# Performance work log

Hardware: AMD Instinct MI355X
Metric: run time of the kernel (lower is better)

## Reference

```python
import jax, jax.numpy as jnp
import numpy as np

THRESH = 1.0
TAU_M = 20.0
TAU_S = 5.0
NUM_STEPS = 8
SCALE = 0.2
BATCH = 8
DM = np.float32(np.exp(-1.0 / TAU_M))
DS = np.float32(np.exp(-1.0 / TAU_S))


@jax.custom_vjp
def spike_fn(x):
    return (x > 0.0).astype(x.dtype)

def _sf_fwd(x):
    return (x > 0.0).astype(x.dtype), x

def _sf_bwd(x, g):
    # rectangular surrogate gradient (lens = 0.5), standard for NOSO/SNN training
    return (g * (jnp.abs(x) < 0.5).astype(x.dtype),)

spike_fn.defvjp(_sf_fwd, _sf_bwd)


def conv5x5(x, w):
    return jax.lax.conv_general_dilated(x, w, (1, 1), ((2, 2), (2, 2)),
                                        dimension_numbers=('NCHW', 'OIHW', 'NCHW'))


def noso_conv(w, in_sp, sav, vm, vs):
    # dual-exponential NOSO neuron: pre-synaptic traces vm/vs, membrane u = sav*(conv(vm)-conv(vs))
    vm = DM * vm + in_sp
    vs = DS * vs + in_sp
    um = conv5x5(vm, w)
    us = conv5x5(vs, w)
    u = sav * (um - us)
    sp = spike_fn(u - THRESH)
    sav = sav * (1.0 - sp)  # one spike per neuron
    return sav, vm, vs, um, u, sp


def noso_fc(w, in_sp, sav, vm, vs):
    vm = DM * vm + in_sp
    vs = DS * vs + in_sp
    um = jnp.einsum('bi,oi->bo', vm, w)
    us = jnp.einsum('bi,oi->bo', vs, w)
    u = sav * (um - us)
    sp = spike_fn(u - THRESH)
    sav = sav * (1.0 - sp)
    return sav, vm, vs, um, u, sp


def minpool(sp, lat):
    # latency-based 2x2 min-pool: pass through the spike whose neuron fired earliest
    b, c, h, w = sp.shape
    s = sp.reshape(b, c, h // 2, 2, w // 2, 2).transpose(0, 1, 2, 4, 3, 5).reshape(b, c, h // 2, w // 2, 4)
    l = lat.reshape(b, c, h // 2, 2, w // 2, 2).transpose(0, 1, 2, 4, 3, 5).reshape(b, c, h // 2, w // 2, 4)
    idx = jnp.argmin(l, axis=-1)
    return jnp.take_along_axis(s, idx[..., None], axis=-1)[..., 0]


def xavier(key, shape, fan_in, fan_out):
    a = np.float32(np.sqrt(6.0 / (fan_in + fan_out)))
    return jax.random.uniform(key, shape, jnp.float32, -a, a)


def setup_inputs():
    key = jax.random.key(0)
    ks = jax.random.split(key, 9)
    inp = {'input': jax.random.uniform(ks[0], (BATCH, 3, 32, 32), jnp.float32)}
    def cw(k, o, i):
        return xavier(k, (o, i, 5, 5), i * 25, o * 25)
    def lw(k, o, i):
        return xavier(k, (o, i), i, o)
    inp['wc1'] = cw(ks[1], 64, 3)
    inp['wc2'] = cw(ks[2], 128, 64)
    inp['wc3'] = cw(ks[3], 256, 128)
    inp['wc4'] = cw(ks[4], 512, 256)
    inp['wc5'] = cw(ks[5], 256, 512)
    inp['wf1'] = lw(ks[6], 1024, 16384)
    inp['wf2'] = lw(ks[7], 512, 1024)
    inp['wf3'] = lw(ks[8], 10, 512)
    inp['batch_size'] = BATCH
    return inp


def forward(input, wc1, wc2, wc3, wc4, wc5, wf1, wf2, wf3, batch_size):
    B = batch_size
    f32 = jnp.float32
    def Z(*s):
        return jnp.zeros((B,) + s, f32)
    def O(*s):
        return jnp.ones((B,) + s, f32)
    carry = {
        'in_u': Z(3, 32, 32),
        'h1': (O(64, 32, 32), Z(3, 32, 32), Z(3, 32, 32)),
        'h2': (O(128, 32, 32), Z(64, 32, 32), Z(64, 32, 32)),
        'h3': (O(256, 16, 16), Z(128, 16, 16), Z(128, 16, 16)),
        'h4': (O(512, 8, 8), Z(256, 8, 8), Z(256, 8, 8)),
        'h5': (O(256, 8, 8), Z(512, 8, 8), Z(512, 8, 8)),
        'f1': (O(1024), Z(16384), Z(16384)),
        'f2': (O(512), Z(1024), Z(1024)),
        'f3': (O(10), Z(512), Z(512)),
        'p1e': Z(128, 32, 32),
        'p1l': float(NUM_STEPS) * O(128, 32, 32),
        'p2e': Z(256, 16, 16),
        'p2l': float(NUM_STEPS) * O(256, 16, 16),
        'te': Z(10),
        'out_t': float(NUM_STEPS) * O(10),
        'out_u': Z(10),
        'sum_sp': jnp.zeros((9,), f32),
    }

    def step(c, _):
        # input encoding neuron (thresh=1, leaky integrate + reset on spike)
        in_u = DM * c['in_u'] + input * SCALE
        in_sp = spike_fn(in_u - 1.0)
        in_u = in_u * (1.0 - in_sp)
        s1, vm1, vs1, um1, u1, sp1 = noso_conv(wc1, in_sp, *c['h1'])
        s2, vm2, vs2, um2, u2, sp2 = noso_conv(wc2, sp1, *c['h2'])
        p1e = c['p1e'] + ((c['p1e'] + (um2 != 0).astype(f32)) != 0).astype(f32)
        p1l = c['p1l'] + jax.lax.stop_gradient(sp2) * (p1e - NUM_STEPS + 1.0)
        s3, vm3, vs3, um3, u3, sp3 = noso_conv(wc3, minpool(sp2, p1l), *c['h3'])
        p2e = c['p2e'] + ((c['p2e'] + (um3 != 0).astype(f32)) != 0).astype(f32)
        p2l = c['p2l'] + jax.lax.stop_gradient(sp3) * (p2e - NUM_STEPS + 1.0)
        s4, vm4, vs4, um4, u4, sp4 = noso_conv(wc4, minpool(sp3, p2l), *c['h4'])
        s5, vm5, vs5, um5, u5, sp5 = noso_conv(wc5, sp4, *c['h5'])
        sf1, vmf1, vsf1, umf1, uf1, spf1 = noso_fc(wf1, sp5.reshape(B, -1), *c['f1'])
        sf2, vmf2, vsf2, umf2, uf2, spf2 = noso_fc(wf2, spf1, *c['f2'])
        sf3, vmf3, vsf3, umf3, uf3, spf3 = noso_fc(wf3, spf2, *c['f3'])
        te = c['te'] + ((c['te'] + (uf3 != 0).astype(f32)) != 0).astype(f32)
        out_t = c['out_t'] + spf3 * jax.lax.stop_gradient(te - NUM_STEPS)  # dodt forward
        out_u = c['out_u'] + spf3 * uf3
        sum_sp = c['sum_sp'] + jnp.stack([in_sp.sum(), sp1.sum(), sp2.sum(), sp3.sum(),
                                          sp4.sum(), sp5.sum(), spf1.sum(), spf2.sum(), spf3.sum()])
        nc = {'in_u': in_u,
              'h1': (s1, vm1, vs1), 'h2': (s2, vm2, vs2), 'h3': (s3, vm3, vs3),
              'h4': (s4, vm4, vs4), 'h5': (s5, vm5, vs5),
              'f1': (sf1, vmf1, vsf1), 'f2': (sf2, vmf2, vsf2), 'f3': (sf3, vmf3, vsf3),
              'p1e': p1e, 'p1l': p1l, 'p2e': p2e, 'p2l': p2l,
              'te': te, 'out_t': out_t, 'out_u': out_u, 'sum_sp': sum_sp}
        return nc, None

    c, _ = jax.lax.scan(step, carry, None, length=NUM_STEPS)
    return c['out_t'], c['out_u'], c['sum_sp']


def reference(input, wc1, wc2, wc3, wc4, wc5, wf1, wf2, wf3, batch_size):
    return forward(input, wc1, wc2, wc3, wc4, wc5, wf1, wf2, wf3, batch_size)
```

## Files before the change

kernel.cpp:

```cpp
#include <hip/hip_runtime.h>
#include <cstddef>

#define B 8
constexpr int TAIL_NB = 256;

constexpr float DM = 0.95122942450071400910f;
constexpr float DS = 0.81873075307798185867f;

constexpr int BS_L0 = 3 * 32 * 32;
constexpr int BS_L1 = 64 * 32 * 32;
constexpr int BS_P1 = 128 * 16 * 16;
constexpr int BS_P2 = 256 * 8 * 8;
constexpr int BS_L4 = 512 * 8 * 8;
constexpr int BS_L5 = 256 * 8 * 8;
constexpr int BS_F1 = 1024;
constexpr int BS_F2 = 512;

constexpr size_t I_L0 = 0;
constexpr size_t I_L1 = I_L0 + 8 * (size_t)B * BS_L0;
constexpr size_t I_P1 = I_L1 + 8 * (size_t)B * BS_L1;
constexpr size_t I_P2 = I_P1 + 8 * (size_t)B * BS_P1;
constexpr size_t I_L4 = I_P2 + 8 * (size_t)B * BS_P2;
constexpr size_t I_L5 = I_L4 + 8 * (size_t)B * BS_L4;
constexpr size_t I_F1 = I_L5 + 8 * (size_t)B * BS_L5;
constexpr size_t I_F2 = I_F1 + 8 * (size_t)B * BS_F1;
constexpr size_t I_CNT = I_F2 + 8 * (size_t)B * BS_F2;
constexpr size_t I_SUMP = I_CNT + 512;
constexpr size_t I_BAR = I_SUMP + 16;
constexpr size_t INT_TOTAL = I_BAR + 2;
constexpr size_t WS_NEED = INT_TOTAL * sizeof(int);

constexpr int ilog2(int n) { int l = 0; while (n > 1) { n >>= 1; ++l; } return l; }

__device__ __forceinline__ int ldcnt(const int* p) {
  return __hip_atomic_load(p, __ATOMIC_RELAXED, __HIP_MEMORY_SCOPE_AGENT);
}

__device__ __forceinline__ void block_stage(bool sp, int idx, int* s_list, int* s_n) {
  unsigned long long bal = __ballot(sp);
  if (bal == 0ull) return;
  int lane = threadIdx.x & 63;
  int leader = (int)__ffsll((unsigned long long)bal) - 1;
  int base = 0;
  if (lane == leader) base = atomicAdd(s_n, __popcll(bal));
  base = __shfl(base, leader);
  if (sp) s_list[base + __popcll(bal & ((1ull << lane) - 1ull))] = idx;
}

__device__ __forceinline__ void wave_append(bool sp, int idx, int* cnt, int* list) {
  unsigned long long bal = __ballot(sp);
  if (bal == 0ull) return;
  int lane = threadIdx.x & 63;
  int leader = (int)__ffsll((unsigned long long)bal) - 1;
  int base = 0;
  if (lane == leader) base = atomicAdd(cnt, __popcll(bal));
  base = __shfl(base, leader);
  if (sp) list[base + __popcll(bal & ((1ull << lane) - 1ull))] = idx;
}

__device__ __forceinline__ bool layer_any(const int* cnt, int ci, int tid, int* s_gate) {
  __syncthreads();
  if (tid == 0) *s_gate = 0;
  __syncthreads();
  if (tid < 64) {
    int t = tid >> 3, b = tid & 7;
    if (ldcnt(cnt + (t * 8 + ci) * 8 + b) > 0) *s_gate = 1;
  }
  __syncthreads();
  return *s_gate != 0;
}

__device__ __forceinline__ void gbar(int* bar, int tid) {
  __threadfence();
  __syncthreads();
  if (tid == 0) {
    int g = __hip_atomic_load(bar + 1, __ATOMIC_RELAXED, __HIP_MEMORY_SCOPE_AGENT);
    int a = __hip_atomic_fetch_add(bar, 1, __ATOMIC_ACQ_REL, __HIP_MEMORY_SCOPE_AGENT);
    if (a == TAIL_NB - 1) {
      __hip_atomic_store(bar, 0, __ATOMIC_RELAXED, __HIP_MEMORY_SCOPE_AGENT);
      __hip_atomic_store(bar + 1, g + 1, __ATOMIC_RELEASE, __HIP_MEMORY_SCOPE_AGENT);
    } else {
      while (__hip_atomic_load(bar + 1, __ATOMIC_ACQUIRE, __HIP_MEMORY_SCOPE_AGENT) == g)
        __builtin_amdgcn_s_sleep(1);
    }
  }
  __syncthreads();
  __threadfence();
}

__global__ __launch_bounds__(512) void k_encode(const float* __restrict__ in,
                                                int* __restrict__ iws) {
  const int tid = threadIdx.x;
  const int b = blockIdx.x;
  int* cnt = iws + I_CNT;
  if (tid < 56) {
    int t = tid / 7, ci = 1 + tid % 7;
    cnt[(t * 8 + ci) * 8 + b] = 0;
  }
  if (b == 0 && tid >= 64 && tid < 82) iws[I_SUMP + (tid - 64)] = 0;
  __shared__ unsigned long long s_bal[48];
  __shared__ int s_off[48];
  const int lane = tid & 63, w = tid >> 6;
  float x[6], u[6];
#pragma unroll
  for (int k = 0; k < 6; ++k) {
    x[k] = in[b * BS_L0 + tid + k * 512] * 0.2f;
    u[k] = 0.0f;
  }
#pragma clang loop unroll(disable)
  for (int t = 0; t < 8; ++t) {
    __syncthreads();
    int spm = 0;
#pragma unroll
    for (int k = 0; k < 6; ++k) {
      u[k] = DM * u[k] + x[k];
      bool sp = (u[k] - 1.0f > 0.0f);
      if (sp) { u[k] = 0.0f; spm |= 1 << k; }
      unsigned long long bal = __ballot(sp);
      if (lane == 0) s_bal[k * 8 + w] = bal;
    }
    __syncthreads();
    if (tid < 48) {
      int v = __popcll(s_bal[tid]);
      int incl = v;
#pragma unroll
      for (int d = 1; d < 64; d <<= 1) {
        int o = __shfl_up(incl, d);
        if (lane >= d) incl += o;
      }
      s_off[tid] = incl - v;
      if (tid == 47) cnt[(t * 8 + 0) * 8 + b] = incl;
    }
    __syncthreads();
    int* list = iws + I_L0 + ((size_t)t * B + b) * BS_L0;
#pragma unroll
    for (int k = 0; k < 6; ++k) {
      if (spm & (1 << k)) {
        int word = k * 8 + w;
        int rank = __popcll(s_bal[word] & ((1ull << lane) - 1ull));
        list[s_off[word] + rank] = tid + k * 512;
      }
    }
  }
}

__global__ __launch_bounds__(256) void k_conv1(const float* __restrict__ w,
                                               int* __restrict__ iws) {
  const int tid = threadIdx.x;
  const int plane = blockIdx.x;
  const int b = plane >> 6;
  const int oc = plane & 63;
  int* cnt = iws + I_CNT;
  __shared__ float s_w[75];
  __shared__ float s_acc[1024];
  __shared__ int s_list[BS_L0];
  __shared__ int s_cnt[8];
  if (tid < 8) s_cnt[tid] = ldcnt(cnt + (tid * 8 + 0) * 8 + b);
  if (tid >= 64 && tid < 139) s_w[tid - 64] = w[oc * 75 + (tid - 64)];
  __syncthreads();
  float um[4], us[4], sav[4];
#pragma unroll
  for (int k = 0; k < 4; ++k) { um[k] = 0.0f; us[k] = 0.0f; sav[k] = 1.0f; }
  bool active = false;
#pragma clang loop unroll(disable)
  for (int t = 0; t < 8; ++t) {
    const int S = s_cnt[t];
    if (!active && S == 0) continue;
    active = true;
#pragma clang loop unroll(disable)
    for (int p = tid; p < 1024; p += 256) s_acc[p] = 0.0f;
    const int* glist = iws + I_L0 + ((size_t)t * B + b) * BS_L0;
#pragma clang loop unroll(disable)
    for (int j = tid; j < S; j += 256) s_list[j] = glist[j];
    __syncthreads();
    const int total = S << 5;
#pragma clang loop unroll(disable)
    for (int i = tid; i < total; i += 256) {
      int k = i & 31;
      if (k < 25) {
        int loc = s_list[i >> 5];
        int c = loc >> 10;
        int p = loc & 1023;
        int ki = (k * 205) >> 10;
        int oy = (p >> 5) + 2 - ki;
        int ox = (p & 31) + 2 - (k - ki * 5);
        if ((unsigned)oy < 32u && (unsigned)ox < 32u)
          atomicAdd(&s_acc[(oy << 5) + ox], s_w[c * 25 + k]);
      }
    }
    __syncthreads();
    int* out_cnt = cnt + (t * 8 + 1) * 8 + b;
    int* out_list = iws + I_L1 + ((size_t)t * B + b) * BS_L1;
#pragma unroll
    for (int k = 0; k < 4; ++k) {
      int p = tid + (k << 8);
      float cv = s_acc[p];
      float m = DM * um[k] + cv;
      float s2 = DS * us[k] + cv;
      um[k] = m;
      us[k] = s2;
      float uu = sav[k] * (m - s2);
      bool sp = (uu - 1.0f > 0.0f);
      if (sp) sav[k] = 0.0f;
      wave_append(sp, (oc << 10) + p, out_cnt, out_list);
    }
    __syncthreads();
  }
}

template <int CIN, int COUT, int H, int W, bool POOL, int PPB, bool WLDS>
__device__ void conv_phase(int bid, int tid, const float* __restrict__ w, int* cnt, int in_ci,
                           int out_ci, const int* __restrict__ in_list0, int in_bs,
                           int* __restrict__ out_list0, int out_bs, float* sump_layer,
                           float* s_acc, float* s_plb, float* s_spb, float* s_w, int* s_list,
                           int* s_n, int* s_base, int* s_uc, int* s_cnt) {
  constexpr int HW = H * W;
  constexpr int HWlog = ilog2(HW);
  constexpr int Wlog = ilog2(W);
  constexpr int PPT = (HW + 255) / 256;
  int wcount = 0;
  const int b = (bid * PPB) >> ilog2(COUT);
  if (tid < 8) s_cnt[tid] = ldcnt(cnt + (tid * 8 + in_ci) * 8 + b);
  __syncthreads();
#pragma clang loop unroll(disable)
  for (int pl = 0; pl < PPB; ++pl) {
    const int plane = bid * PPB + pl;
    const int oc = plane & (COUT - 1);
    if constexpr (WLDS) {
#pragma clang loop unroll(disable)
      for (int j = tid; j < CIN * 25; j += 256) s_w[j] = w[(size_t)oc * CIN * 25 + j];
    }
    float um[PPT], us[PPT], sav[PPT], pe[PPT], plat[PPT];
#pragma unroll
    for (int k = 0; k < PPT; ++k) {
      um[k] = 0.0f; us[k] = 0.0f; sav[k] = 1.0f; pe[k] = 0.0f; plat[k] = 8.0f;
    }
    bool active = false;
#pragma clang loop unroll(disable)
    for (int t = 0; t < 8; ++t) {
      const int S = s_cnt[t];
      if (!active && S == 0) continue;
      active = true;
#pragma clang loop unroll(disable)
      for (int p = tid; p < HW; p += 256) s_acc[p] = 0.0f;
      if (tid == 0) *s_n = 0;
      __syncthreads();
      const int* list = in_list0 + ((size_t)t * B + b) * in_bs;
#pragma clang loop unroll(disable)
      for (int s = tid; s < S; s += 256) {
        int loc = list[s];
        int c = loc >> HWlog;
        int p = loc & (HW - 1);
        int y = p >> Wlog, x = p & (W - 1);
        const float* wp = WLDS ? (const float*)s_w + c * 25 : w + ((size_t)oc * CIN + c) * 25;
#pragma clang loop unroll(disable)
        for (int ki = 0; ki < 5; ++ki) {
          int oy = y + 2 - ki;
          if ((unsigned)oy < (unsigned)H) {
#pragma clang loop unroll(disable)
            for (int kj = 0; kj < 5; ++kj) {
              int ox = x + 2 - kj;
              if ((unsigned)ox < (unsigned)W) atomicAdd(&s_acc[oy * W + ox], wp[ki * 5 + kj]);
            }
          }
        }
      }
      __syncthreads();
#pragma unroll
      for (int k = 0; k < PPT; ++k) {
        int p = tid + k * 256;
        bool lane_ok = (p < HW);
        float cv = lane_ok ? s_acc[p] : 0.0f;
        float m = DM * um[k] + cv;
        float s2 = DS * us[k] + cv;
        um[k] = m;
        us[k] = s2;
        float uu = sav[k] * (m - s2);
        bool sp = lane_ok && (uu - 1.0f > 0.0f);
        if (sp) sav[k] = 0.0f;
        if constexpr (POOL) {
          unsigned long long bal = __ballot(sp);
          if ((tid & 63) == 0) wcount += (int)__popcll(bal);
          if (lane_ok) {
            float act = (m != 0.0f) ? 1.0f : 0.0f;
            float pen = pe[k] + (((pe[k] + act) != 0.0f) ? 1.0f : 0.0f);
            pe[k] = pen;
            if (sp) plat[k] += pen - 7.0f;
            s_plb[p] = plat[k];
            s_spb[p] = sp ? 1.0f : 0.0f;
          }
        } else {
          block_stage(sp, (oc << HWlog) + p, s_list, s_n);
        }
      }
      __syncthreads();
      if constexpr (POOL) {
        constexpr int HP = H / 2, WP = W / 2;
#pragma clang loop unroll(disable)
        for (int q = tid; q < HP * WP; q += 256) {
          int py = q / WP, px = q - py * WP;
          int base = (2 * py) * W + 2 * px;
          float l0 = s_plb[base], l1 = s_plb[base + 1], l2 = s_plb[base + W],
                l3 = s_plb[base + W + 1];
          int off = 0;
          float lm = l0;
          if (l1 < lm) { lm = l1; off = 1; }
          if (l2 < lm) { lm = l2; off = W; }
          if (l3 < lm) { lm = l3; off = W + 1; }
          bool psp = (s_spb[base + off] != 0.0f);
          block_stage(psp, oc * (HP * WP) + q, s_list, s_n);
        }
        __syncthreads();
      }
      if (tid == 0 && *s_n > 0) *s_base = atomicAdd(cnt + (t * 8 + out_ci) * 8 + b, *s_n);
      __syncthreads();
      int* out_list = out_list0 + ((size_t)t * B + b) * out_bs;
      int n = *s_n;
#pragma clang loop unroll(disable)
      for (int j = tid; j < n; j += 256) out_list[*s_base + j] = s_list[j];
      __syncthreads();
    }
  }
  if constexpr (POOL) {
    if (tid == 0) *s_uc = 0;
    __syncthreads();
    if ((tid & 63) == 0 && wcount) atomicAdd(s_uc, wcount);
    __syncthreads();
    if (tid == 0 && *s_uc) atomicAdd(sump_layer + b, (float)*s_uc);
  }
}

template <int IN, int OUT>
__device__ void fc_phase(int bid, int tid, const float* __restrict__ w, int* cnt, int in_ci,
                         int out_ci, const int* __restrict__ in_list0, int in_bs,
                         int* __restrict__ out_list0, int out_bs, int* s_list, int* s_n,
                         int* s_base, int* s_cnt) {
  const int q = bid * 256 + tid;
  const int b = q >> ilog2(OUT);
  const int o = q & (OUT - 1);
  if (tid < 8) s_cnt[tid] = ldcnt(cnt + (tid * 8 + in_ci) * 8 + b);
  __syncthreads();
  float um = 0.0f, us = 0.0f, sav = 1.0f;
  bool active = false;
#pragma clang loop unroll(disable)
  for (int t = 0; t < 8; ++t) {
    const int S = s_cnt[t];
    if (!active && S == 0) continue;
    active = true;
    if (tid == 0) *s_n = 0;
    __syncthreads();
    const int* list = in_list0 + ((size_t)t * B + b) * in_bs;
    float acc = 0.0f;
#pragma clang loop unroll(disable)
    for (int s = 0; s < S; ++s) acc += w[(size_t)o * IN + list[s]];
    float m = DM * um + acc;
    float s2 = DS * us + acc;
    um = m;
    us = s2;
    float uu = sav * (m - s2);
    bool sp = (uu - 1.0f > 0.0f);
    if (sp) sav = 0.0f;
    block_stage(sp, o, s_list, s_n);
    __syncthreads();
    if (tid == 0 && *s_n > 0) *s_base = atomicAdd(cnt + (t * 8 + out_ci) * 8 + b, *s_n);
    __syncthreads();
    int* out_list = out_list0 + ((size_t)t * B + b) * out_bs;
    int n = *s_n;
#pragma clang loop unroll(disable)
    for (int j = tid; j < n; j += 256) out_list[*s_base + j] = s_list[j];
    __syncthreads();
  }
}

__device__ void fc3_phase(int tid, const float* __restrict__ w, const int* cnt, int in_ci,
                          const int* __restrict__ in_list0, int in_bs,
                          const float* __restrict__ sump, float* __restrict__ out, int* s_c3) {
  if (tid == 0) *s_c3 = 0;
  __syncthreads();
  const bool lane_ok = (tid < 80);
  const int b = lane_ok ? tid / 10 : 0;
  const int o = lane_ok ? tid - b * 10 : 0;
  float um = 0.0f, us = 0.0f, sav = 1.0f, te = 0.0f, ot = 8.0f, ou = 0.0f;
  bool active = false;
#pragma clang loop unroll(disable)
  for (int t = 0; t < 8; ++t) {
    const int S = lane_ok ? ldcnt(cnt + (t * 8 + in_ci) * 8 + b) : 0;
    if (!active && !__any(S > 0)) continue;
    active = true;
    const int* list = in_list0 + ((size_t)t * B + b) * in_bs;
    float acc = 0.0f;
#pragma clang loop unroll(disable)
    for (int s = 0; s < S; ++s) acc += w[o * 512 + list[s]];
    float m = DM * um + acc;
    float s2 = DS * us + acc;
    um = m;
    us = s2;
    float uu = sav * (m - s2);
    bool sp = lane_ok && (uu - 1.0f > 0.0f);
    if (sp) sav = 0.0f;
    float act = (uu != 0.0f) ? 1.0f : 0.0f;
    te = te + (((te + act) != 0.0f) ? 1.0f : 0.0f);
    if (sp) {
      ot += te - 8.0f;
      ou += uu;
    }
    unsigned long long bal = __ballot(sp);
    if ((tid & 63) == 0 && bal) atomicAdd(s_c3, (int)__popcll(bal));
  }
  if (tid < 80) {
    out[tid] = ot;
    out[80 + tid] = ou;
  }
  __syncthreads();
  if (tid < 8) {
    float s = 0.0f;
    if (tid == 2 || tid == 3) {
      const float* sp = sump + (tid - 2) * 8;
      for (int b2 = 0; b2 < 8; ++b2) s += sp[b2];
    } else {
      for (int t = 0; t < 8; ++t)
        for (int b2 = 0; b2 < 8; ++b2) s += (float)cnt[(t * 8 + tid) * 8 + b2];
    }
    out[160 + tid] = s;
  }
  if (tid == 0) out[168] = (float)*s_c3;
}

__global__ __launch_bounds__(256) void k_tail(const float* __restrict__ wc2,
                                              const float* __restrict__ wc3,
                                              const float* __restrict__ wc4,
                                              const float* __restrict__ wc5,
                                              const float* __restrict__ wf1,
                                              const float* __restrict__ wf2,
                                              const float* __restrict__ wf3,
                                              float* __restrict__ out, int* __restrict__ iws) {
  __shared__ float s_w[3200];
  __shared__ float s_acc[1024];
  __shared__ float s_plb[1024];
  __shared__ float s_spb[1024];
  __shared__ int s_list[1024];
  __shared__ int s_n, s_base, s_uc, s_gate, s_c3, s_cnt[8];
  const int tid = threadIdx.x;
  const int bid = blockIdx.x;
  int* cnt = iws + I_CNT;
  float* sump = (float*)(iws + I_SUMP);
  int* bar = iws + I_BAR;

  if (layer_any(cnt, 1, tid, &s_gate)) {
    conv_phase<64, 128, 32, 32, true, 4, true>(bid, tid, wc2, cnt, 1, 2, iws + I_L1, BS_L1,
                                               iws + I_P1, BS_P1, sump + 0, s_acc, s_plb, s_spb,
                                               s_w, s_list, &s_n, &s_base, &s_uc, s_cnt);
    gbar(bar, tid);
  }
  if (layer_any(cnt, 2, tid, &s_gate)) {
    conv_phase<128, 256, 16, 16, true, 8, true>(bid, tid, wc3, cnt, 2, 3, iws + I_P1, BS_P1,
                                                iws + I_P2, BS_P2, sump + 8, s_acc, s_plb, s_spb,
                                                s_w, s_list, &s_n, &s_base, &s_uc, s_cnt);
    gbar(bar, tid);
  }
  if (layer_any(cnt, 3, tid, &s_gate)) {
    conv_phase<256, 512, 8, 8, false, 16, false>(bid, tid, wc4, cnt, 3, 4, iws + I_P2, BS_P2,
                                                 iws + I_L4, BS_L4, nullptr, s_acc, s_plb, s_spb,
                                                 s_w, s_list, &s_n, &s_base, &s_uc, s_cnt);
    gbar(bar, tid);
  }
  if (layer_any(cnt, 4, tid, &s_gate)) {
    conv_phase<512, 256, 8, 8, false, 8, false>(bid, tid, wc5, cnt, 4, 5, iws + I_L4, BS_L4,
                                                iws + I_L5, BS_L5, nullptr, s_acc, s_plb, s_spb,
                                                s_w, s_list, &s_n, &s_base, &s_uc, s_cnt);
    gbar(bar, tid);
  }
  if (layer_any(cnt, 5, tid, &s_gate)) {
    if (bid < B * 1024 / 256)
      fc_phase<16384, 1024>(bid, tid, wf1, cnt, 5, 6, iws + I_L5, BS_L5, iws + I_F1, BS_F1,
                            s_list, &s_n, &s_base, s_cnt);
    gbar(bar, tid);
  }
  if (layer_any(cnt, 6, tid, &s_gate)) {
    if (bid < B * 512 / 256)
      fc_phase<1024, 512>(bid, tid, wf2, cnt, 6, 7, iws + I_F1, BS_F1, iws + I_F2, BS_F2,
                          s_list, &s_n, &s_base, s_cnt);
    gbar(bar, tid);
  }
  if (bid == 0)
    fc3_phase(tid, wf3, cnt, 7, iws + I_F2, BS_F2, sump, out, &s_c3);
}

extern "C" void kernel_launch(void* const* d_in, const int* in_sizes, int n_in, void* d_out,
                              int out_size, void* d_ws, size_t ws_size, hipStream_t stream) {
  const float* input = (const float*)d_in[0];
  const float* wc1 = (const float*)d_in[1];
  const float* wc2 = (const float*)d_in[2];
  const float* wc3 = (const float*)d_in[3];
  const float* wc4 = (const float*)d_in[4];
  const float* wc5 = (const float*)d_in[5];
  const float* wf1 = (const float*)d_in[6];
  const float* wf2 = (const float*)d_in[7];
  const float* wf3 = (const float*)d_in[8];
  float* out = (float*)d_out;
  int* iws = (int*)d_ws;
  if (ws_size < WS_NEED) return;

  k_encode<<<B, 512, 0, stream>>>(input, iws);
  k_conv1<<<512, 256, 0, stream>>>(wc1, iws);
  k_tail<<<TAIL_NB, 256, 0, stream>>>(wc2, wc3, wc4, wc5, wf1, wf2, wf3, out, iws);
}
```

Baseline: 74.17 us.

## Batch all timesteps in encode and conv1 to remove per-step barriers

The encoder now computes spikes for all 8 timesteps first, stores ballots per timestep, and runs the prefix scans for all timesteps in parallel (one wave per step) before writing the lists. conv1 moves to 1024-thread blocks, accumulates all timesteps into separate shared-memory planes with no barrier between steps, reads input lists straight from global memory instead of staging them in LDS, and then runs the neuron recurrence once per pixel at the end. The aim is to cut the many __syncthreads per timestep and add parallelism. In exchange it uses 32KB of LDS per block, which may limit occupancy, and gives up skipping the accumulator reset for inactive steps.

```diff
diff --git a/kernel.cpp b/kernel.cpp
--- a/kernel.cpp
+++ b/kernel.cpp
@@ -98,8 +98,8 @@
     cnt[(t * 8 + ci) * 8 + b] = 0;
   }
   if (b == 0 && tid >= 64 && tid < 82) iws[I_SUMP + (tid - 64)] = 0;
-  __shared__ unsigned long long s_bal[48];
-  __shared__ int s_off[48];
+  __shared__ unsigned long long s_bal[8 * 48];
+  __shared__ int s_off[8 * 48];
   const int lane = tid & 63, w = tid >> 6;
   float x[6], u[6];
 #pragma unroll
@@ -107,104 +107,96 @@
     x[k] = in[b * BS_L0 + tid + k * 512] * 0.2f;
     u[k] = 0.0f;
   }
-#pragma clang loop unroll(disable)
-  for (int t = 0; t < 8; ++t) {
-    __syncthreads();
-    int spm = 0;
+  unsigned long long spmall = 0ull;
+#pragma clang loop unroll(disable)
+  for (int t = 0; t < 8; ++t) {
 #pragma unroll
     for (int k = 0; k < 6; ++k) {
       u[k] = DM * u[k] + x[k];
       bool sp = (u[k] - 1.0f > 0.0f);
-      if (sp) { u[k] = 0.0f; spm |= 1 << k; }
+      if (sp) { u[k] = 0.0f; spmall |= 1ull << (t * 6 + k); }
       unsigned long long bal = __ballot(sp);
-      if (lane == 0) s_bal[k * 8 + w] = bal;
-    }
-    __syncthreads();
-    if (tid < 48) {
-      int v = __popcll(s_bal[tid]);
-      int incl = v;
-#pragma unroll
-      for (int d = 1; d < 64; d <<= 1) {
-        int o = __shfl_up(incl, d);
-        if (lane >= d) incl += o;
+      if (lane == 0) s_bal[t * 48 + k * 8 + w] = bal;
+    }
+  }
+  __syncthreads();
+  if (lane < 48) {
+    const int t = w;
+    int v = __popcll(s_bal[t * 48 + lane]);
+    int incl = v;
+#pragma unroll
+    for (int d = 1; d < 64; d <<= 1) {
+      int o = __shfl_up(incl, d);
+      if (lane >= d) incl += o;
+    }
+    s_off[t * 48 + lane] = incl - v;
+    if (lane == 47) cnt[(t * 8 + 0) * 8 + b] = incl;
+  }
+  __syncthreads();
+#pragma clang loop unroll(disable)
+  for (int t = 0; t < 8; ++t) {
+    int* list = iws + I_L0 + ((size_t)t * B + b) * BS_L0;
+#pragma unroll
+    for (int k = 0; k < 6; ++k) {
+      if (spmall & (1ull << (t * 6 + k))) {
+        int word = k * 8 + w;
+        int rank = __popcll(s_bal[t * 48 + word] & ((1ull << lane) - 1ull));
+        list[s_off[t * 48 + word] + rank] = tid + k * 512;
       }
-      s_off[tid] = incl - v;
-      if (tid == 47) cnt[(t * 8 + 0) * 8 + b] = incl;
-    }
-    __syncthreads();
-    int* list = iws + I_L0 + ((size_t)t * B + b) * BS_L0;
-#pragma unroll
-    for (int k = 0; k < 6; ++k) {
-      if (spm & (1 << k)) {
-        int word = k * 8 + w;
-        int rank = __popcll(s_bal[word] & ((1ull << lane) - 1ull));
-        list[s_off[word] + rank] = tid + k * 512;
-      }
-    }
-  }
-}
-
-__global__ __launch_bounds__(256) void k_conv1(const float* __restrict__ w,
-                                               int* __restrict__ iws) {
+    }
+  }
+}
+
+__global__ __launch_bounds__(1024) void k_conv1(const float* __restrict__ w,
+                                                int* __restrict__ iws) {
   const int tid = threadIdx.x;
   const int plane = blockIdx.x;
   const int b = plane >> 6;
   const int oc = plane & 63;
   int* cnt = iws + I_CNT;
+  __shared__ float s_acc[8 * 1024];
   __shared__ float s_w[75];
-  __shared__ float s_acc[1024];
-  __shared__ int s_list[BS_L0];
   __shared__ int s_cnt[8];
   if (tid < 8) s_cnt[tid] = ldcnt(cnt + (tid * 8 + 0) * 8 + b);
   if (tid >= 64 && tid < 139) s_w[tid - 64] = w[oc * 75 + (tid - 64)];
-  __syncthreads();
-  float um[4], us[4], sav[4];
-#pragma unroll
-  for (int k = 0; k < 4; ++k) { um[k] = 0.0f; us[k] = 0.0f; sav[k] = 1.0f; }
-  bool active = false;
+#pragma unroll
+  for (int t = 0; t < 8; ++t) s_acc[t * 1024 + tid] = 0.0f;
+  __syncthreads();
 #pragma clang loop unroll(disable)
   for (int t = 0; t < 8; ++t) {
     const int S = s_cnt[t];
-    if (!active && S == 0) continue;
-    active = true;
-#pragma clang loop unroll(disable)
-    for (int p = tid; p < 1024; p += 256) s_acc[p] = 0.0f;
+    if (S == 0) continue;
     const int* glist = iws + I_L0 + ((size_t)t * B + b) * BS_L0;
-#pragma clang loop unroll(disable)
-    for (int j = tid; j < S; j += 256) s_list[j] = glist[j];
-    __syncthreads();
     const int total = S << 5;
 #pragma clang loop unroll(disable)
-    for (int i = tid; i < total; i += 256) {
+    for (int i = tid; i < total; i += 1024) {
       int k = i & 31;
       if (k < 25) {
-        int loc = s_list[i >> 5];
+        int loc = glist[i >> 5];
         int c = loc >> 10;
         int p = loc & 1023;
         int ki = (k * 205) >> 10;
         int oy = (p >> 5) + 2 - ki;
         int ox = (p & 31) + 2 - (k - ki * 5);
         if ((unsigned)oy < 32u && (unsigned)ox < 32u)
-          atomicAdd(&s_acc[(oy << 5) + ox], s_w[c * 25 + k]);
+          atomicAdd(&s_acc[t * 1024 + (oy << 5) + ox], s_w[c * 25 + k]);
       }
     }
-    __syncthreads();
-    int* out_cnt = cnt + (t * 8 + 1) * 8 + b;
-    int* out_list = iws + I_L1 + ((size_t)t * B + b) * BS_L1;
-#pragma unroll
-    for (int k = 0; k < 4; ++k) {
-      int p = tid + (k << 8);
-      float cv = s_acc[p];
-      float m = DM * um[k] + cv;
-      float s2 = DS * us[k] + cv;
-      um[k] = m;
-      us[k] = s2;
-      float uu = sav[k] * (m - s2);
-      bool sp = (uu - 1.0f > 0.0f);
-      if (sp) sav[k] = 0.0f;
-      wave_append(sp, (oc << 10) + p, out_cnt, out_list);
-    }
-    __syncthreads();
+  }
+  __syncthreads();
+  float um = 0.0f, us = 0.0f, sav = 1.0f;
+#pragma clang loop unroll(disable)
+  for (int t = 0; t < 8; ++t) {
+    float cv = s_acc[t * 1024 + tid];
+    float m = DM * um + cv;
+    float s2 = DS * us + cv;
+    um = m;
+    us = s2;
+    float uu = sav * (m - s2);
+    bool sp = (uu - 1.0f > 0.0f);
+    if (sp) sav = 0.0f;
+    wave_append(sp, (oc << 10) + tid, cnt + (t * 8 + 1) * 8 + b,
+                iws + I_L1 + ((size_t)t * B + b) * BS_L1);
   }
 }
 
@@ -502,6 +494,6 @@
   if (ws_size < WS_NEED) return;
 
   k_encode<<<B, 512, 0, stream>>>(input, iws);
-  k_conv1<<<512, 256, 0, stream>>>(wc1, iws);
+  k_conv1<<<512, 1024, 0, stream>>>(wc1, iws);
   k_tail<<<TAIL_NB, 256, 0, stream>>>(wc2, wc3, wc4, wc5, wf1, wf2, wf3, out, iws);
 }
```

Measured after the change: 67.69 us (median of 2 runs). 1.1x faster.
